# Kernel optimization log

Measured on AMD Instinct MI355X. Metric: run time of the kernel, lower is better.

## Reference

```python
import jax, jax.numpy as jnp
import numpy as np

B, TA, TV, D, H = 4, 1024, 1024, 512, 8
HD = D // H
SCALE = HD ** -0.5
LN_EPS = 1e-5


def setup_inputs() -> dict:
    key = jax.random.key(0)
    ks = jax.random.split(key, 16)
    init = lambda k, shape, s: (jax.random.normal(k, shape, jnp.float32) * s)
    inp = {
        'q': jax.random.normal(ks[0], (B, TA, D), jnp.float32),
        'k': jax.random.normal(ks[1], (B, TV, D), jnp.float32),
        'v': jax.random.normal(ks[2], (B, TV, D), jnp.float32),
        'guide_map': jax.random.uniform(ks[3], (B, TA, TV), jnp.float32),
        'Wq': init(ks[4], (D, D), D ** -0.5), 'bq': jnp.zeros((D,), jnp.float32),
        'Wk': init(ks[5], (D, D), D ** -0.5), 'bk': jnp.zeros((D,), jnp.float32),
        'Wv': init(ks[6], (D, D), D ** -0.5), 'bv': jnp.zeros((D,), jnp.float32),
        'Wo': init(ks[7], (D, D), D ** -0.5), 'bo': jnp.zeros((D,), jnp.float32),
        'ln_gamma': jnp.ones((D,), jnp.float32),
        'ln_beta': jnp.zeros((D,), jnp.float32),
        'gate': jnp.zeros((1,), jnp.float32),
        'bias_scale': jnp.array(10.0, jnp.float32),
    }
    return inp


def layer_norm(x, gamma, beta):
    mu = jnp.mean(x, axis=-1, keepdims=True)
    var = jnp.mean(jnp.square(x - mu), axis=-1, keepdims=True)
    return (x - mu) * jax.lax.rsqrt(var + LN_EPS) * gamma + beta


def reference(q, k, v, guide_map, Wq, bq, Wk, bk, Wv, bv, Wo, bo, ln_gamma, ln_beta, gate, bias_scale):
    # project and split heads: [B, H, T, hd]
    Q = (q @ Wq.T + bq).reshape(B, TA, H, HD).transpose(0, 2, 1, 3)
    K = (k @ Wk.T + bk).reshape(B, TV, H, HD).transpose(0, 2, 1, 3)
    V = (v @ Wv.T + bv).reshape(B, TV, H, HD).transpose(0, 2, 1, 3)
    scores = jnp.einsum('bhqd,bhkd->bhqk', Q, K) * SCALE
    # transport bias, broadcast over heads (guide_map is [B,Ta,Tv])
    transport_bias = jnp.log(guide_map + 1e-8) * jax.nn.softplus(bias_scale)
    scores = scores + transport_bias[:, None, :, :]
    attn = jax.nn.softmax(scores, axis=-1)  # dropout is identity in eval
    context = jnp.einsum('bhqk,bhkd->bhqd', attn, V)
    context = context.transpose(0, 2, 1, 3).reshape(B, TA, D)
    out = context @ Wo.T + bo
    return layer_norm(q + jax.nn.sigmoid(gate) * out, ln_gamma, ln_beta)
```

## Files before the change

kernel.cpp:

```cpp
#include <hip/hip_runtime.h>
#include <hip/hip_bf16.h>
#include <math.h>

typedef __bf16 bf16_t;
typedef _Float16 hf16_t;
typedef bf16_t bf16x8 __attribute__((ext_vector_type(8)));
typedef bf16_t bf16x4 __attribute__((ext_vector_type(4)));
typedef hf16_t hf16x8 __attribute__((ext_vector_type(8)));
typedef float f32x4 __attribute__((ext_vector_type(4)));
typedef short s16x4 __attribute__((ext_vector_type(4)));

#define B_  4
#define TA_ 1024
#define TV_ 1024
#define D_  512
#define H_  8
#define HD_ 64
#define SCALE_ 0.125f
#define LOG2E_ 1.442695041f
#define QSCALE_ 0.1803368801f
#define DEFER_THR_ 11.5416f

__device__ inline float fast_exp2(float x) { return __builtin_amdgcn_exp2f(x); }

__device__ inline void g2l16(const void* g, void* l) {
    __builtin_amdgcn_global_load_lds(
        (const __attribute__((address_space(1))) void*)g,
        (__attribute__((address_space(3))) void*)l, 16, 0, 0);
}

__device__ inline f32x4 mfma16_bf16(bf16x4 a, bf16x4 b, f32x4 c) {
    return __builtin_amdgcn_mfma_f32_16x16x16bf16_1k(
        __builtin_bit_cast(s16x4, a), __builtin_bit_cast(s16x4, b), c, 0, 0, 0);
}

__global__ __launch_bounds__(256) void prep_all(
    const float* __restrict__ G, hf16_t* __restrict__ bias_t,
    const float* __restrict__ q, const float* __restrict__ k, const float* __restrict__ v,
    const float* __restrict__ Wq, const float* __restrict__ Wk,
    const float* __restrict__ Wv, const float* __restrict__ Wo,
    bf16_t* __restrict__ qb, bf16_t* __restrict__ kb, bf16_t* __restrict__ vb,
    bf16_t* __restrict__ Wb)
{
    const int tid = threadIdx.x;
    if (blockIdx.x < 1024) {
        __shared__ float Gt[64][68];
        const int kt = blockIdx.x & 15, q64 = (blockIdx.x >> 4) & 15, b = blockIdx.x >> 8;
        const int row = tid >> 4, col4 = (tid & 15) * 4;
        #pragma unroll
        for (int it = 0; it < 4; ++it) {
            int r = it * 16 + row;
            f32x4 g = *(const f32x4*)(G + ((size_t)(b * TA_ + q64 * 64 + r)) * TV_ + kt * 64 + col4);
            *(f32x4*)&Gt[r][col4] = g;
        }
        __syncthreads();
        const int lane = tid & 63, wave = tid >> 6, quad = lane >> 4, l16 = lane & 15;
        hf16x8 lo, hi;
        #pragma unroll
        for (int ct = 0; ct < 4; ++ct) {
            #pragma unroll
            for (int r = 0; r < 4; ++r) {
                float gv = Gt[wave * 16 + l16][ct * 16 + quad * 4 + r];
                float lb = __logf(gv + 1e-8f);
                int idx = ct * 4 + r;
                if (idx < 8) lo[idx] = (hf16_t)lb; else hi[idx - 8] = (hf16_t)lb;
            }
        }
        size_t doff = ((((size_t)b * 16 + kt) * 16 + q64) * 256 + tid) * 16;
        *(hf16x8*)(bias_t + doff) = lo;
        *(hf16x8*)(bias_t + doff + 8) = hi;
    } else {
        const size_t i = ((size_t)(blockIdx.x - 1024) * 256 + tid) * 8;
        const float* src; bf16_t* dst; size_t off;
        const size_t M2 = (size_t)1 << 21;
        if (i < M2)          { src = q; dst = qb; off = i; }
        else if (i < 2 * M2) { src = k; dst = kb; off = i - M2; }
        else if (i < 3 * M2) { src = v; dst = vb; off = i - 2 * M2; }
        else {
            size_t j = i - 3 * M2;
            int wsel = (int)(j >> 18); off = j & 262143;
            src = (wsel == 0) ? Wq : (wsel == 1) ? Wk : (wsel == 2) ? Wv : Wo;
            dst = Wb + ((size_t)wsel << 18);
        }
        f32x4 a = *(const f32x4*)(src + off), c = *(const f32x4*)(src + off + 4);
        bf16x8 r;
        #pragma unroll
        for (int t = 0; t < 4; ++t) { r[t] = (bf16_t)a[t]; r[t + 4] = (bf16_t)c[t]; }
        *(bf16x8*)(dst + off) = r;
    }
}

__global__ __launch_bounds__(256) void gemm_qkv(
    const bf16_t* __restrict__ qb, const bf16_t* __restrict__ kb, const bf16_t* __restrict__ vb,
    const bf16_t* __restrict__ Wb,
    const float* __restrict__ bq, const float* __restrict__ bk, const float* __restrict__ bv,
    bf16_t* __restrict__ Qp, bf16_t* __restrict__ Kp, bf16_t* __restrict__ Vt)
{
    __shared__ bf16_t Asm[2][128 * 32];
    __shared__ bf16_t Bsm[2][64 * 32];

    const int tid  = threadIdx.x;
    const int wave = tid >> 6, lane = tid & 63;
    const int quad = lane >> 4, l16 = lane & 15;
    const int wm = wave & 1, wn = wave >> 1;
    const int mbase = blockIdx.x * 128, nbase = blockIdx.y * 64;
    const int z = blockIdx.z;
    const int srow = lane >> 2;
    const int scol = (lane & 3) * 8;

    const bf16_t* X   = (z == 0) ? qb : (z == 1) ? kb : vb;
    const float* bias = (z == 0) ? bq : (z == 1) ? bk : bv;
    const bf16_t* W   = Wb + ((size_t)z << 18);

    auto stage = [&](int kt, int buf) {
        const int k0 = kt * 32;
        #pragma unroll
        for (int i = 0; i < 2; ++i) {
            const int row = wave * 32 + i * 16;
            g2l16(X + (size_t)(mbase + row + srow) * D_ + k0 + scol,
                  &Asm[buf][row * 32] + (size_t)lane * 8);
        }
        {
            const int row = wave * 16;
            g2l16(W + (size_t)(nbase + row + srow) * D_ + k0 + scol,
                  &Bsm[buf][row * 32] + (size_t)lane * 8);
        }
    };

    f32x4 acc[4][2] = {};
    stage(0, 0);
    __syncthreads();
    for (int kt = 0; kt < 16; ++kt) {
        const int buf = kt & 1;
        if (kt < 15) stage(kt + 1, buf ^ 1);
        bf16x8 af[4], bf_[2];
        #pragma unroll
        for (int t = 0; t < 4; ++t)
            af[t]  = *(const bf16x8*)&Asm[buf][(wm * 64 + t * 16 + l16) * 32 + quad * 8];
        #pragma unroll
        for (int t = 0; t < 2; ++t)
            bf_[t] = *(const bf16x8*)&Bsm[buf][(wn * 32 + t * 16 + l16) * 32 + quad * 8];
        #pragma unroll
        for (int mt = 0; mt < 4; ++mt) {
            #pragma unroll
            for (int nt = 0; nt < 2; ++nt)
                acc[mt][nt] = __builtin_amdgcn_mfma_f32_16x16x32_bf16(af[mt], bf_[nt], acc[mt][nt], 0, 0, 0);
        }
        __syncthreads();
    }

    bf16_t* out = (z == 0) ? Qp : (z == 1) ? Kp : Vt;
    #pragma unroll
    for (int mt = 0; mt < 4; ++mt) {
        #pragma unroll
        for (int nt = 0; nt < 2; ++nt) {
            const int n = nbase + wn * 32 + nt * 16 + l16;
            const float bn = bias[n];
            if (z == 2) {
                int m0 = mbase + wm * 64 + mt * 16 + quad * 4;
                int b = m0 >> 10, t = m0 & 1023, h = n >> 6, hd = n & 63;
                bf16x4 pk;
                #pragma unroll
                for (int r = 0; r < 4; ++r) pk[r] = (bf16_t)(acc[mt][nt][r] + bn);
                *(bf16x4*)(out + ((size_t)(b * H_ + h) * HD_ + hd) * TV_ + t) = pk;
            } else {
                #pragma unroll
                for (int r = 0; r < 4; ++r) {
                    int m = mbase + wm * 64 + mt * 16 + quad * 4 + r;
                    float val = acc[mt][nt][r] + bn;
                    if (z == 0) val *= QSCALE_;
                    int b = m >> 10, t = m & 1023, h = n >> 6, hd = n & 63;
                    out[(((size_t)(b * H_ + h) * TA_) + t) * HD_ + hd] = (bf16_t)val;
                }
            }
        }
    }
}

__global__ __launch_bounds__(512, 4) void attn_kernel(
    const bf16_t* __restrict__ Qp, const bf16_t* __restrict__ Kp,
    const bf16_t* __restrict__ Vt, const hf16_t* __restrict__ bias_t,
    const float* __restrict__ bias_scale, bf16_t* __restrict__ ctx)
{
    __shared__ bf16_t Ksm[2][2][64][72];
    __shared__ bf16_t Vsm[2][2][64][76];

    const int tid  = threadIdx.x;
    const int wave = tid >> 6, lane = tid & 63;
    const int half = wave >> 2, w4 = wave & 3;
    const int quad = lane >> 4, l16 = lane & 15;
    const int bh = blockIdx.x, b = bh >> 3, h = bh & 7;
    const int q64 = blockIdx.y;
    const int t0 = half * 8;
    const int qbase = q64 * 64 + w4 * 16;
    const int rsub = lane >> 3, csub = lane & 7;
    const int shsrc = (lane & 48) | ((lane >> 2) & 12);

    const float sp = log1pf(__expf(bias_scale[0])) * LOG2E_;

    bf16x8 aq[2];
    #pragma unroll
    for (int s = 0; s < 2; ++s)
        aq[s] = *(const bf16x8*)(Qp + ((size_t)bh * TA_ + qbase + l16) * HD_ + s * 32 + quad * 8);

    f32x4 o[4] = {};
    float m_ = -1e30f, l_ = 0.f;

    auto issue_kv = [&](int kt, bf16x8 kr[2], bf16x8 vr[2]) {
        const int kbase = kt * 64;
        #pragma unroll
        for (int i = 0; i < 2; ++i) {
            int row = w4 * 16 + i * 8 + rsub;
            kr[i] = *(const bf16x8*)(Kp + ((size_t)bh * TV_ + kbase + row) * HD_ + csub * 8);
            vr[i] = *(const bf16x8*)(Vt + ((size_t)bh * HD_ + row) * TV_ + kbase + csub * 8);
        }
    };
    auto write_kv = [&](int buf, bf16x8 kr[2], bf16x8 vr[2]) {
        #pragma unroll
        for (int i = 0; i < 2; ++i) {
            int row = w4 * 16 + i * 8 + rsub;
            *(bf16x8*)&Ksm[half][buf][row][(csub ^ (row & 7)) * 8] = kr[i];
            *(bf16x4*)&Vsm[half][buf][row][csub * 8]     = *(const bf16x4*)&vr[i];
            *(bf16x4*)&Vsm[half][buf][row][csub * 8 + 4] = *((const bf16x4*)&vr[i] + 1);
        }
    };

    const int tidb = (w4 << 6) | lane;
    const hf16_t* bias_base = bias_t + (((size_t)b * 16 * 16 + q64) * 256 + tidb) * 16;
    auto bias_ld = [&](int kt, hf16x8& lo, hf16x8& hi) {
        const hf16_t* bp = bias_base + (size_t)kt * 65536;
        lo = *(const hf16x8*)bp;
        hi = *(const hf16x8*)(bp + 8);
    };
    hf16x8 b0lo, b0hi, b1lo, b1hi;
    bias_ld(t0, b0lo, b0hi);
    bias_ld(t0 + 1, b1lo, b1hi);

    {
        bf16x8 kr[2], vr[2];
        issue_kv(t0, kr, vr);
        write_kv(0, kr, vr);
    }
    __syncthreads();

    auto tile_body = [&](int lk, int buf, hf16x8& slo, hf16x8& shi) {
        const int kt = t0 + lk;
        bf16x8 krn[2], vrn[2];
        if (lk < 7) issue_kv(kt + 1, krn, vrn);
        hf16x8 clo = slo, chi = shi;
        if (lk < 6) bias_ld(kt + 2, slo, shi);

        f32x4 st[4];
        __builtin_amdgcn_s_setprio(1);
        #pragma unroll
        for (int ct = 0; ct < 4; ++ct) {
            f32x4 acc = {};
            #pragma unroll
            for (int s = 0; s < 2; ++s) {
                bf16x8 bk = *(const bf16x8*)&Ksm[half][buf][ct * 16 + l16]
                                                 [((4 * s + quad) ^ (l16 & 7)) * 8];
                acc = __builtin_amdgcn_mfma_f32_16x16x32_bf16(bk, aq[s], acc, 0, 0, 0);
            }
            st[ct] = acc;
        }
        __builtin_amdgcn_s_setprio(0);
        float sv[4][4], mx = -1e30f;
        #pragma unroll
        for (int ct = 0; ct < 4; ++ct) {
            #pragma unroll
            for (int r = 0; r < 4; ++r) {
                int idx = ct * 4 + r;
                float lb = (idx < 8) ? (float)clo[idx] : (float)chi[idx - 8];
                float val = fmaf(lb, sp, st[ct][r]);
                sv[ct][r] = val;
                mx = fmaxf(mx, val);
            }
        }
        mx = fmaxf(mx, __shfl_xor(mx, 16, 64));
        mx = fmaxf(mx, __shfl_xor(mx, 32, 64));
        float mn;
        if (__all(mx - m_ <= DEFER_THR_)) {
            mn = m_;
        } else {
            mn = fmaxf(m_, mx);
            float alpha = fast_exp2(m_ - mn);
            m_ = mn;
            l_ *= alpha;
            #pragma unroll
            for (int r = 0; r < 4; ++r) {
                float af = __shfl(alpha, shsrc | r, 64);
                #pragma unroll
                for (int dt = 0; dt < 4; ++dt) o[dt][r] *= af;
            }
        }
        float ls = 0.f;
        #pragma unroll
        for (int ct = 0; ct < 4; ++ct) {
            #pragma unroll
            for (int r = 0; r < 4; ++r) {
                float p = fast_exp2(sv[ct][r] - mn);
                sv[ct][r] = p;
                ls += p;
            }
        }
        ls += __shfl_xor(ls, 16, 64);
        ls += __shfl_xor(ls, 32, 64);
        l_ += ls;
        if (lk < 7) write_kv(buf ^ 1, krn, vrn);
        __builtin_amdgcn_s_setprio(1);
        #pragma unroll
        for (int ct = 0; ct < 4; ++ct) {
            bf16x4 ap;
            #pragma unroll
            for (int r = 0; r < 4; ++r) ap[r] = (bf16_t)sv[ct][r];
            #pragma unroll
            for (int dt = 0; dt < 4; ++dt) {
                bf16x4 bv = *(const bf16x4*)&Vsm[half][buf][dt * 16 + l16][ct * 16 + quad * 4];
                o[dt] = mfma16_bf16(ap, bv, o[dt]);
            }
        }
        __builtin_amdgcn_s_setprio(0);
        __syncthreads();
    };

    #pragma unroll 1
    for (int kk = 0; kk < 8; kk += 2) {
        tile_body(kk,     0, b0lo, b0hi);
        tile_body(kk + 1, 1, b1lo, b1hi);
    }

    float* cb = (float*)&Ksm[0][0][0][0];
    if (half == 1) {
        float* p = cb + (size_t)tidb * 18;
        #pragma unroll
        for (int dt = 0; dt < 4; ++dt) {
            #pragma unroll
            for (int r = 0; r < 4; ++r) p[dt * 4 + r] = o[dt][r];
        }
        p[16] = m_; p[17] = l_;
    }
    __syncthreads();
    if (half == 0) {
        const float* p = cb + (size_t)tidb * 18;
        float s0[4], s1[4];
        #pragma unroll
        for (int r = 0; r < 4; ++r) {
            float m0 = __shfl(m_, shsrc | r, 64);
            float l0 = __shfl(l_, shsrc | r, 64);
            const float* pr = cb + (size_t)((w4 << 6) | (shsrc | r)) * 18;
            float m1 = pr[16], l1 = pr[17];
            float mm = fmaxf(m0, m1);
            float e0 = fast_exp2(m0 - mm), e1 = fast_exp2(m1 - mm);
            float L = l0 * e0 + l1 * e1;
            s0[r] = e0 / L; s1[r] = e1 / L;
        }
        #pragma unroll
        for (int dt = 0; dt < 4; ++dt) {
            #pragma unroll
            for (int r = 0; r < 4; ++r) {
                float v = o[dt][r] * s0[r] + p[dt * 4 + r] * s1[r];
                int qrow = q64 * 64 + w4 * 16 + quad * 4 + r;
                ctx[((size_t)b * TA_ + qrow) * D_ + h * HD_ + dt * 16 + l16] = (bf16_t)v;
            }
        }
    }
}

__global__ __launch_bounds__(512) void gemm_out_ln(
    const bf16_t* __restrict__ ctx, const bf16_t* __restrict__ Wob,
    const float* __restrict__ bo, const float* __restrict__ q,
    const float* __restrict__ gamma, const float* __restrict__ beta,
    const float* __restrict__ gate, float* __restrict__ y)
{
    __shared__ bf16_t Asm[2][16 * 32];
    __shared__ bf16_t Bsm[2][512 * 32];
    __shared__ float ps[16][8], psq[16][8];

    const int tid  = threadIdx.x;
    const int wave = tid >> 6, lane = tid & 63;
    const int quad = lane >> 4, l16 = lane & 15;
    const int mbase = blockIdx.x * 16;

    auto stage = [&](int kt, int buf) {
        const int k0 = kt * 32;
        #pragma unroll
        for (int j = 0; j < 4; ++j) {
            int row0 = wave * 64 + j * 16;
            g2l16(Wob + (size_t)(row0 + (lane >> 2)) * D_ + k0 + (lane & 3) * 8,
                  &Bsm[buf][row0 * 32] + (size_t)lane * 8);
        }
        if (wave == 0) {
            g2l16(ctx + (size_t)(mbase + (lane >> 2)) * D_ + k0 + (lane & 3) * 8,
                  &Asm[buf][0] + (size_t)lane * 8);
        }
    };

    f32x4 acc[4] = {};
    stage(0, 0);
    __syncthreads();
    for (int kt = 0; kt < 16; ++kt) {
        const int buf = kt & 1;
        if (kt < 15) stage(kt + 1, buf ^ 1);
        bf16x8 af = *(const bf16x8*)&Asm[buf][l16 * 32 + quad * 8];
        #pragma unroll
        for (int nt = 0; nt < 4; ++nt) {
            bf16x8 bf_ = *(const bf16x8*)&Bsm[buf][(wave * 64 + nt * 16 + l16) * 32 + quad * 8];
            acc[nt] = __builtin_amdgcn_mfma_f32_16x16x32_bf16(af, bf_, acc[nt], 0, 0, 0);
        }
        __syncthreads();
    }

    const float sg = 1.f / (1.f + __expf(-gate[0]));
    float s[4] = {0.f, 0.f, 0.f, 0.f}, sq[4] = {0.f, 0.f, 0.f, 0.f};
    #pragma unroll
    for (int nt = 0; nt < 4; ++nt) {
        int n = wave * 64 + nt * 16 + l16;
        float bon = bo[n];
        #pragma unroll
        for (int r = 0; r < 4; ++r) {
            int m = mbase + quad * 4 + r;
            float x = q[(size_t)m * D_ + n] + sg * (acc[nt][r] + bon);
            acc[nt][r] = x;
            s[r] += x; sq[r] += x * x;
        }
    }
    #pragma unroll
    for (int off = 1; off < 16; off <<= 1) {
        #pragma unroll
        for (int r = 0; r < 4; ++r) {
            s[r]  += __shfl_xor(s[r],  off, 64);
            sq[r] += __shfl_xor(sq[r], off, 64);
        }
    }
    if (l16 == 0) {
        #pragma unroll
        for (int r = 0; r < 4; ++r) {
            ps[quad * 4 + r][wave]  = s[r];
            psq[quad * 4 + r][wave] = sq[r];
        }
    }
    __syncthreads();
    float mu[4], rstd[4];
    #pragma unroll
    for (int r = 0; r < 4; ++r) {
        int row = quad * 4 + r;
        float S = 0.f, SQ = 0.f;
        #pragma unroll
        for (int wv = 0; wv < 8; ++wv) { S += ps[row][wv]; SQ += psq[row][wv]; }
        mu[r] = S * (1.f / D_);
        float var = SQ * (1.f / D_) - mu[r] * mu[r];
        rstd[r] = rsqrtf(var + 1e-5f);
    }
    #pragma unroll
    for (int nt = 0; nt < 4; ++nt) {
        int n = wave * 64 + nt * 16 + l16;
        float gn = gamma[n], bn = beta[n];
        #pragma unroll
        for (int r = 0; r < 4; ++r) {
            int m = mbase + quad * 4 + r;
            y[(size_t)m * D_ + n] = (acc[nt][r] - mu[r]) * rstd[r] * gn + bn;
        }
    }
}

extern "C" void kernel_launch(void* const* d_in, const int* in_sizes, int n_in,
                              void* d_out, int out_size, void* d_ws, size_t ws_size,
                              hipStream_t stream) {
    const float* q       = (const float*)d_in[0];
    const float* k       = (const float*)d_in[1];
    const float* v       = (const float*)d_in[2];
    const float* guide   = (const float*)d_in[3];
    const float* Wq      = (const float*)d_in[4];
    const float* bq      = (const float*)d_in[5];
    const float* Wk      = (const float*)d_in[6];
    const float* bk      = (const float*)d_in[7];
    const float* Wv      = (const float*)d_in[8];
    const float* bv      = (const float*)d_in[9];
    const float* Wo      = (const float*)d_in[10];
    const float* bo      = (const float*)d_in[11];
    const float* gamma   = (const float*)d_in[12];
    const float* beta    = (const float*)d_in[13];
    const float* gate    = (const float*)d_in[14];
    const float* bscale  = (const float*)d_in[15];

    char* w = (char*)d_ws;
    bf16_t* qb     = (bf16_t*)(w);
    bf16_t* kb     = (bf16_t*)(w + (4u  << 20));
    bf16_t* vb     = (bf16_t*)(w + (8u  << 20));
    bf16_t* Wb     = (bf16_t*)(w + (12u << 20));
    bf16_t* Qp     = (bf16_t*)(w + (14u << 20));
    bf16_t* Kp     = (bf16_t*)(w + (18u << 20));
    bf16_t* Vt     = (bf16_t*)(w + (22u << 20));
    bf16_t* ctx    = (bf16_t*)(w + (26u << 20));
    hf16_t* bias_t = (hf16_t*)(w + (30u << 20));

    prep_all<<<4608, 256, 0, stream>>>(guide, bias_t, q, k, v, Wq, Wk, Wv, Wo, qb, kb, vb, Wb);
    gemm_qkv<<<dim3(32, 8, 3), 256, 0, stream>>>(qb, kb, vb, Wb, bq, bk, bv, Qp, Kp, Vt);
    attn_kernel<<<dim3(32, 16), 512, 0, stream>>>(Qp, Kp, Vt, bias_t, bscale, ctx);
    gemm_out_ln<<<256, 512, 0, stream>>>(ctx, Wb + ((size_t)3 << 18), bo, q,
                                         gamma, beta, gate, (float*)d_out);
}
```

Before: 170.4 us.

## Move guide-map log-bias computation from prep kernel into QKV GEMM launch

The log-bias transform of the guide map moves out of the conversion kernel and into extra blocks of the QKV projection GEMM launch, which is flattened to a 1D grid sharing one raw shared-memory buffer. This aims to overlap the memory-bound bias work with the compute-bound GEMM and to shorten the prep kernel. The cost is a larger, heterogeneous grid. The bias blocks sit after the GEMM blocks, so they may just trail behind rather than truly overlap.

```diff
diff --git a/kernel.cpp b/kernel.cpp
--- a/kernel.cpp
+++ b/kernel.cpp
@@ -35,7 +35,6 @@
 }
 
 __global__ __launch_bounds__(256) void prep_all(
-    const float* __restrict__ G, hf16_t* __restrict__ bias_t,
     const float* __restrict__ q, const float* __restrict__ k, const float* __restrict__ v,
     const float* __restrict__ Wq, const float* __restrict__ Wk,
     const float* __restrict__ Wv, const float* __restrict__ Wo,
@@ -43,9 +42,39 @@
     bf16_t* __restrict__ Wb)
 {
     const int tid = threadIdx.x;
-    if (blockIdx.x < 1024) {
-        __shared__ float Gt[64][68];
-        const int kt = blockIdx.x & 15, q64 = (blockIdx.x >> 4) & 15, b = blockIdx.x >> 8;
+    const size_t i = ((size_t)blockIdx.x * 256 + tid) * 8;
+    const float* src; bf16_t* dst; size_t off;
+    const size_t M2 = (size_t)1 << 21;
+    if (i < M2)          { src = q; dst = qb; off = i; }
+    else if (i < 2 * M2) { src = k; dst = kb; off = i - M2; }
+    else if (i < 3 * M2) { src = v; dst = vb; off = i - 2 * M2; }
+    else {
+        size_t j = i - 3 * M2;
+        int wsel = (int)(j >> 18); off = j & 262143;
+        src = (wsel == 0) ? Wq : (wsel == 1) ? Wk : (wsel == 2) ? Wv : Wo;
+        dst = Wb + ((size_t)wsel << 18);
+    }
+    f32x4 a = *(const f32x4*)(src + off), c = *(const f32x4*)(src + off + 4);
+    bf16x8 r;
+    #pragma unroll
+    for (int t = 0; t < 4; ++t) { r[t] = (bf16_t)a[t]; r[t + 4] = (bf16_t)c[t]; }
+    *(bf16x8*)(dst + off) = r;
+}
+
+__global__ __launch_bounds__(256) void gemm_qkv(
+    const bf16_t* __restrict__ qb, const bf16_t* __restrict__ kb, const bf16_t* __restrict__ vb,
+    const bf16_t* __restrict__ Wb,
+    const float* __restrict__ bq, const float* __restrict__ bk, const float* __restrict__ bv,
+    bf16_t* __restrict__ Qp, bf16_t* __restrict__ Kp, bf16_t* __restrict__ Vt,
+    const float* __restrict__ G, hf16_t* __restrict__ bias_t)
+{
+    __shared__ __align__(16) char smem[24576];
+    const int tid  = threadIdx.x;
+
+    if (blockIdx.x >= 768) {
+        float (*Gt)[68] = (float(*)[68])smem;
+        const int bx = blockIdx.x - 768;
+        const int kt = bx & 15, q64 = (bx >> 4) & 15, b = bx >> 8;
         const int row = tid >> 4, col4 = (tid & 15) * 4;
         #pragma unroll
         for (int it = 0; it < 4; ++it) {
@@ -69,42 +98,18 @@
         size_t doff = ((((size_t)b * 16 + kt) * 16 + q64) * 256 + tid) * 16;
         *(hf16x8*)(bias_t + doff) = lo;
         *(hf16x8*)(bias_t + doff + 8) = hi;
-    } else {
-        const size_t i = ((size_t)(blockIdx.x - 1024) * 256 + tid) * 8;
-        const float* src; bf16_t* dst; size_t off;
-        const size_t M2 = (size_t)1 << 21;
-        if (i < M2)          { src = q; dst = qb; off = i; }
-        else if (i < 2 * M2) { src = k; dst = kb; off = i - M2; }
-        else if (i < 3 * M2) { src = v; dst = vb; off = i - 2 * M2; }
-        else {
-            size_t j = i - 3 * M2;
-            int wsel = (int)(j >> 18); off = j & 262143;
-            src = (wsel == 0) ? Wq : (wsel == 1) ? Wk : (wsel == 2) ? Wv : Wo;
-            dst = Wb + ((size_t)wsel << 18);
-        }
-        f32x4 a = *(const f32x4*)(src + off), c = *(const f32x4*)(src + off + 4);
-        bf16x8 r;
-        #pragma unroll
-        for (int t = 0; t < 4; ++t) { r[t] = (bf16_t)a[t]; r[t + 4] = (bf16_t)c[t]; }
-        *(bf16x8*)(dst + off) = r;
-    }
-}
-
-__global__ __launch_bounds__(256) void gemm_qkv(
-    const bf16_t* __restrict__ qb, const bf16_t* __restrict__ kb, const bf16_t* __restrict__ vb,
-    const bf16_t* __restrict__ Wb,
-    const float* __restrict__ bq, const float* __restrict__ bk, const float* __restrict__ bv,
-    bf16_t* __restrict__ Qp, bf16_t* __restrict__ Kp, bf16_t* __restrict__ Vt)
-{
-    __shared__ bf16_t Asm[2][128 * 32];
-    __shared__ bf16_t Bsm[2][64 * 32];
-
-    const int tid  = threadIdx.x;
+        return;
+    }
+
+    bf16_t (*Asm)[128 * 32] = (bf16_t(*)[128 * 32])smem;
+    bf16_t (*Bsm)[64 * 32]  = (bf16_t(*)[64 * 32])(smem + 16384);
+
     const int wave = tid >> 6, lane = tid & 63;
     const int quad = lane >> 4, l16 = lane & 15;
     const int wm = wave & 1, wn = wave >> 1;
-    const int mbase = blockIdx.x * 128, nbase = blockIdx.y * 64;
-    const int z = blockIdx.z;
+    const int bx = blockIdx.x;
+    const int z = bx >> 8, rem = bx & 255;
+    const int mbase = (rem & 31) * 128, nbase = (rem >> 5) * 64;
     const int srow = lane >> 2;
     const int scol = (lane & 3) * 8;
 
@@ -494,8 +499,9 @@
     bf16_t* ctx    = (bf16_t*)(w + (26u << 20));
     hf16_t* bias_t = (hf16_t*)(w + (30u << 20));
 
-    prep_all<<<4608, 256, 0, stream>>>(guide, bias_t, q, k, v, Wq, Wk, Wv, Wo, qb, kb, vb, Wb);
-    gemm_qkv<<<dim3(32, 8, 3), 256, 0, stream>>>(qb, kb, vb, Wb, bq, bk, bv, Qp, Kp, Vt);
+    prep_all<<<3584, 256, 0, stream>>>(q, k, v, Wq, Wk, Wv, Wo, qb, kb, vb, Wb);
+    gemm_qkv<<<1792, 256, 0, stream>>>(qb, kb, vb, Wb, bq, bk, bv, Qp, Kp, Vt,
+                                       guide, bias_t);
     attn_kernel<<<dim3(32, 16), 512, 0, stream>>>(Qp, Kp, Vt, bias_t, bscale, ctx);
     gemm_out_ln<<<256, 512, 0, stream>>>(ctx, Wb + ((size_t)3 << 18), bo, q,
                                          gamma, beta, gate, (float*)d_out);
```

Result: no change. 167.7 us (-1.6%).
